# Performance work log

Measured on AMD Instinct MI355X. Metric: run time of the kernel, lower is better.

Reference implementation:

```python
import jax, jax.numpy as jnp
import numpy as np

N, E, D = 50000, 1600000, 64


def setup_inputs() -> dict:
    key = jax.random.key(0)
    ks = jax.random.split(key, 10)
    s = 1.0 / np.sqrt(D)
    return {
        "x": jax.random.normal(ks[0], (N, D), dtype=jnp.float32),
        "edge_index": jax.random.randint(ks[1], (2, E), 0, N, dtype=jnp.int64),
        "edge_weight": jax.random.uniform(ks[2], (E,), dtype=jnp.float32),
        "W_rel1": jax.random.uniform(ks[3], (D, D), jnp.float32, -s, s),
        "b_rel1": jax.random.uniform(ks[4], (D,), jnp.float32, -s, s),
        "W_root1": jax.random.uniform(ks[5], (D, D), jnp.float32, -s, s),
        "W_rel2": jax.random.uniform(ks[6], (D, D), jnp.float32, -s, s),
        "b_rel2": jax.random.uniform(ks[7], (D,), jnp.float32, -s, s),
        "W_root2": jax.random.uniform(ks[8], (D, D), jnp.float32, -s, s),
    }


def graph_conv(x, src, dst, edge_weight, W_rel, b_rel, W_root):
    # message: edge_weight * x[src]; aggregate: sum into dst
    msg = edge_weight[:, None] * x[src]                      # [E, D]
    agg = jax.ops.segment_sum(msg, dst, num_segments=x.shape[0])  # [N, D]
    return agg @ W_rel.T + b_rel + x @ W_root.T


def reference(x, edge_index, edge_weight, W_rel1, b_rel1, W_root1, W_rel2, b_rel2, W_root2):
    src, dst = edge_index[0], edge_index[1]
    h = jax.nn.relu(graph_conv(x, src, dst, edge_weight, W_rel1, b_rel1, W_root1))
    # dropout is identity in eval mode
    h = jax.nn.relu(graph_conv(h, src, dst, edge_weight, W_rel2, b_rel2, W_root2))
    return h
```

## Files before the change

### kernel.cpp

```cpp
#include <hip/hip_runtime.h>


#define NN 50000
#define DD 64
#define EE 1600000
#define NPB 64
#define NB  ((NN + NPB - 1) / NPB)
#define PAD 2560
#define CHUNK 4096
#define NC ((EE + CHUNK - 1) / CHUNK)

static_assert(NC <= 512, "colscan 2-per-thread scan covers <=512 chunks");
static_assert(NB <= 1024, "LDS cursor arrays sized for NB");

typedef __attribute__((ext_vector_type(8))) short short8;
typedef __attribute__((ext_vector_type(4))) float f32x4;

__device__ __forceinline__ unsigned short f2bf(float f) {
    unsigned u = __float_as_uint(f);
    u += 0x7FFF + ((u >> 16) & 1);
    return (unsigned short)(u >> 16);
}
__device__ __forceinline__ float bflo(unsigned u) {
    return __uint_as_float(u << 16);
}
__device__ __forceinline__ float bfhi(unsigned u) {
    return __uint_as_float(u & 0xFFFF0000u);
}
__device__ __forceinline__ unsigned char f2fp8(float f) {
    unsigned p = __builtin_amdgcn_cvt_pk_fp8_f32(f, f, 0, false);
    return (unsigned char)(p & 0xFF);
}

#define XS_STR 72
#define WS_STR 72

__device__ __forceinline__ void transform_body_f32(
    int blk, int t,
    const float* __restrict__ xin,
    const float* __restrict__ Wrel, const float* __restrict__ Wroot,
    const float* __restrict__ bias,
    unsigned char* __restrict__ Z8, unsigned short* __restrict__ Yb,
    unsigned short* Xs, unsigned short* Ws)
{
    const int node0 = blk * 64;

#pragma unroll
    for (int i = 0; i < 8; ++i) {
        int flat = i * 256 + t;
        int row  = flat >> 4;
        int c4   = flat & 15;
        const float* src = (row < 64 ? Wrel + row * 64
                                     : Wroot + (row - 64) * 64) + c4 * 4;
        float4 v = *(const float4*)src;
        unsigned short* d = &Ws[row * WS_STR + c4 * 4];
        d[0] = f2bf(v.x); d[1] = f2bf(v.y); d[2] = f2bf(v.z); d[3] = f2bf(v.w);
    }
#pragma unroll
    for (int i = 0; i < 4; ++i) {
        int flat = i * 256 + t;
        int row  = flat >> 4;
        int c4   = flat & 15;
        int node = node0 + row;
        float4 v = make_float4(0.f, 0.f, 0.f, 0.f);
        if (node < NN) v = *(const float4*)(xin + (size_t)node * 64 + c4 * 4);
        unsigned short* d = &Xs[row * XS_STR + c4 * 4];
        d[0] = f2bf(v.x); d[1] = f2bf(v.y); d[2] = f2bf(v.z); d[3] = f2bf(v.w);
    }
    __syncthreads();

    const int w    = t >> 6;
    const int lane = t & 63;
    const int l15  = lane & 15;
    const int quad = lane >> 4;

    short8 a0 = *(const short8*)&Xs[(w * 16 + l15) * XS_STR + quad * 8];
    short8 a1 = *(const short8*)&Xs[(w * 16 + l15) * XS_STR + 32 + quad * 8];

#pragma unroll
    for (int f = 0; f < 8; ++f) {
        short8 b0 = *(const short8*)&Ws[(f * 16 + l15) * WS_STR + quad * 8];
        short8 b1 = *(const short8*)&Ws[(f * 16 + l15) * WS_STR + 32 + quad * 8];
        f32x4 acc = {0.f, 0.f, 0.f, 0.f};
        acc = __builtin_amdgcn_mfma_f32_16x16x32_bf16(a0, b0, acc, 0, 0, 0);
        acc = __builtin_amdgcn_mfma_f32_16x16x32_bf16(a1, b1, acc, 0, 0, 0);
        const int col = f * 16 + l15;
#pragma unroll
        for (int r = 0; r < 4; ++r) {
            int node = node0 + w * 16 + quad * 4 + r;
            if (node < NN) {
                if (col < 64) Z8[(size_t)node * 64 + col] = f2fp8(acc[r]);
                else          Yb[(size_t)node * 64 + (col - 64)] =
                                  f2bf(acc[r] + bias[col - 64]);
            }
        }
    }
}

__global__ __launch_bounds__(256) void hist_t1_kernel(
    const int* __restrict__ ei, int* __restrict__ hist,
    const float* __restrict__ x,
    const float* __restrict__ Wrel, const float* __restrict__ Wroot,
    const float* __restrict__ bias,
    unsigned char* __restrict__ Z8, unsigned short* __restrict__ Yb)
{
    __shared__ int lh[NB];
    __shared__ unsigned short Xs[64 * XS_STR];
    __shared__ unsigned short Ws[128 * WS_STR];
    const int t = threadIdx.x;

    if (blockIdx.x < NC) {
        const int c = blockIdx.x;
        for (int b = t; b < NB; b += 256) lh[b] = 0;
        __syncthreads();
        const int base = c * CHUNK;
#pragma unroll 4
        for (int i = 0; i < CHUNK; i += 256) {
            int e = base + i + t;
            if (e < EE) atomicAdd(&lh[ei[EE + e] >> 6], 1);
        }
        __syncthreads();
        for (int b = t; b < NB; b += 256) hist[c * NB + b] = lh[b];
    } else {
        transform_body_f32(blockIdx.x - NC, t, x, Wrel, Wroot, bias,
                           Z8, Yb, Xs, Ws);
    }
}

__global__ __launch_bounds__(256) void colscan_wconv_kernel(
    const int* __restrict__ hist, int* __restrict__ offs, int* __restrict__ bsz,
    const float* __restrict__ Wrel2, const float* __restrict__ Wroot2,
    unsigned short* __restrict__ Wb2)
{
    const int t = threadIdx.x;
    if (blockIdx.x >= NB) {
        const int b2 = blockIdx.x - NB;
#pragma unroll
        for (int i = 0; i < 4; ++i) {
            int flat = b2 * 1024 + i * 256 + t;
            int row  = flat >> 4;
            int c4   = flat & 15;
            const float* src = (row < 64 ? Wrel2 + row * 64
                                         : Wroot2 + (row - 64) * 64) + c4 * 4;
            float4 v = *(const float4*)src;
            unsigned short* d = &Wb2[row * 64 + c4 * 4];
            d[0] = f2bf(v.x); d[1] = f2bf(v.y); d[2] = f2bf(v.z); d[3] = f2bf(v.w);
        }
        return;
    }
    __shared__ int part[256];
    const int b = blockIdx.x;
    const int c0 = 2 * t, c1 = 2 * t + 1;
    int h0 = (c0 < NC) ? hist[c0 * NB + b] : 0;
    int h1 = (c1 < NC) ? hist[c1 * NB + b] : 0;
    int pair = h0 + h1;
    part[t] = pair;
    __syncthreads();
    for (int off = 1; off < 256; off <<= 1) {
        int v = (t >= off) ? part[t - off] : 0;
        __syncthreads();
        part[t] += v;
        __syncthreads();
    }
    const int excl = part[t] - pair;
    if (c0 < NC) offs[c0 * NB + b] = b * PAD + excl;
    if (c1 < NC) offs[c1 * NB + b] = b * PAD + excl + h0;
    if (t == 255) bsz[b] = part[255];
}

__global__ __launch_bounds__(512) void bin_kernel(
    const int* __restrict__ ei, const float* __restrict__ ew,
    const int* __restrict__ offs, unsigned* __restrict__ epk)
{
    __shared__ int cur[NB];
    const int c = blockIdx.x, t = threadIdx.x;
    for (int b = t; b < NB; b += 512) cur[b] = offs[c * NB + b];
    __syncthreads();
    const int base = c * CHUNK;
#pragma unroll 4
    for (int i = 0; i < CHUNK; i += 512) {
        int e = base + i + t;
        if (e < EE) {
            int src = ei[e];
            int dst = ei[EE + e];
            unsigned q = (unsigned)fmaf(ew[e], 1023.0f, 0.5f);
            int pos = atomicAdd(&cur[dst >> 6], 1);
            epk[pos] = (unsigned)src | ((unsigned)(dst & 63) << 16) | (q << 22);
        }
    }
}

__global__ __launch_bounds__(512) void aggsort_t2_kernel(
    const unsigned* __restrict__ Z1,
    const uint2* __restrict__ Y4,
    const int* __restrict__ bsz,
    unsigned* __restrict__ epk,
    int* __restrict__ beg, int* __restrict__ endo,
    const unsigned short* __restrict__ Wb2,
    const float* __restrict__ bias2,
    unsigned char* __restrict__ Z8b, unsigned short* __restrict__ Yb2)
{
    __shared__ int      cnt[NPB];
    __shared__ int      nbeg[NPB];
    __shared__ int      cur[NPB];
    __shared__ unsigned stage[PAD];
    __shared__ unsigned short Xs[64 * XS_STR];
    __shared__ unsigned short Ws[128 * WS_STR];
    const int bk = blockIdx.x, t = threadIdx.x;
    const int base = bk * PAD;
    int sz = bsz[bk];
    if (sz > PAD) sz = PAD;

#pragma unroll
    for (int i = 0; i < 2; ++i) {
        int flat = i * 512 + t;
        int row  = flat >> 3;
        int c8   = flat & 7;
        *(short8*)&Ws[row * WS_STR + c8 * 8] =
            *(const short8*)&Wb2[row * 64 + c8 * 8];
    }

    if (t < NPB) cnt[t] = 0;
    __syncthreads();
    for (int i = t; i < sz; i += 512)
        atomicAdd(&cnt[(epk[base + i] >> 16) & 63], 1);
    __syncthreads();

    if (t < 64) {
        int c = cnt[t];
        int v = c;
        for (int off = 1; off < 64; off <<= 1) {
            int u = __shfl_up(v, off);
            if (t >= off) v += u;
        }
        int ex = v - c;
        nbeg[t] = ex;
        cur[t]  = ex;
        int g = bk * NPB + t;
        if (g < NN) { beg[g] = base + ex; endo[g] = base + ex + c; }
    }
    __syncthreads();

    for (int i = t; i < sz; i += 512) {
        unsigned p = epk[base + i];
        int pos = atomicAdd(&cur[(p >> 16) & 63], 1);
        float w = (float)(p >> 22) * (1.0f / 1023.0f);
        stage[pos] = (p & 0xFFFFu) | ((unsigned)f2bf(w) << 16);
    }
    __syncthreads();

    for (int i = t; i < sz; i += 512)
        epk[base + i] = stage[i];

    const int lane = t & 63;
    const int wv   = t >> 6;
    const int s = lane & 15;
    const int q = lane >> 4;

#pragma unroll
    for (int k = 0; k < 8; ++k) {
        const int n6   = wv * 8 + k;
        const int node = bk * 64 + n6;
        const int b = nbeg[n6];
        const int e = b + cnt[n6];
        const uint2 y4 = (node < NN) ? Y4[node * 16 + s] : make_uint2(0u, 0u);

        float a0 = 0.f, a1 = 0.f, a2 = 0.f, a3 = 0.f;
        int i = b;
        for (; i + 16 <= e; i += 16) {
            unsigned pA = stage[i + q];
            unsigned pB = stage[i + 4 + q];
            unsigned pC = stage[i + 8 + q];
            unsigned pD = stage[i + 12 + q];
            unsigned zA = Z1[(pA & 0xFFFF) * 16 + s];
            unsigned zB = Z1[(pB & 0xFFFF) * 16 + s];
            unsigned zC = Z1[(pC & 0xFFFF) * 16 + s];
            unsigned zD = Z1[(pD & 0xFFFF) * 16 + s];
            float wA = __uint_as_float(pA & 0xFFFF0000u);
            float wB = __uint_as_float(pB & 0xFFFF0000u);
            float wC = __uint_as_float(pC & 0xFFFF0000u);
            float wD = __uint_as_float(pD & 0xFFFF0000u);
            a0 = fmaf(wA, __builtin_amdgcn_cvt_f32_fp8(zA, 0), a0);
            a1 = fmaf(wA, __builtin_amdgcn_cvt_f32_fp8(zA, 1), a1);
            a2 = fmaf(wA, __builtin_amdgcn_cvt_f32_fp8(zA, 2), a2);
            a3 = fmaf(wA, __builtin_amdgcn_cvt_f32_fp8(zA, 3), a3);
            a0 = fmaf(wB, __builtin_amdgcn_cvt_f32_fp8(zB, 0), a0);
            a1 = fmaf(wB, __builtin_amdgcn_cvt_f32_fp8(zB, 1), a1);
            a2 = fmaf(wB, __builtin_amdgcn_cvt_f32_fp8(zB, 2), a2);
            a3 = fmaf(wB, __builtin_amdgcn_cvt_f32_fp8(zB, 3), a3);
            a0 = fmaf(wC, __builtin_amdgcn_cvt_f32_fp8(zC, 0), a0);
            a1 = fmaf(wC, __builtin_amdgcn_cvt_f32_fp8(zC, 1), a1);
            a2 = fmaf(wC, __builtin_amdgcn_cvt_f32_fp8(zC, 2), a2);
            a3 = fmaf(wC, __builtin_amdgcn_cvt_f32_fp8(zC, 3), a3);
            a0 = fmaf(wD, __builtin_amdgcn_cvt_f32_fp8(zD, 0), a0);
            a1 = fmaf(wD, __builtin_amdgcn_cvt_f32_fp8(zD, 1), a1);
            a2 = fmaf(wD, __builtin_amdgcn_cvt_f32_fp8(zD, 2), a2);
            a3 = fmaf(wD, __builtin_amdgcn_cvt_f32_fp8(zD, 3), a3);
        }
        for (; i < e; i += 4) {
            int ee = i + q;
            unsigned p = (ee < e) ? stage[ee] : 0u;
            unsigned z = Z1[(p & 0xFFFF) * 16 + s];
            float w = __uint_as_float(p & 0xFFFF0000u);
            a0 = fmaf(w, __builtin_amdgcn_cvt_f32_fp8(z, 0), a0);
            a1 = fmaf(w, __builtin_amdgcn_cvt_f32_fp8(z, 1), a1);
            a2 = fmaf(w, __builtin_amdgcn_cvt_f32_fp8(z, 2), a2);
            a3 = fmaf(w, __builtin_amdgcn_cvt_f32_fp8(z, 3), a3);
        }

        a0 += __shfl_xor(a0, 16); a0 += __shfl_xor(a0, 32);
        a1 += __shfl_xor(a1, 16); a1 += __shfl_xor(a1, 32);
        a2 += __shfl_xor(a2, 16); a2 += __shfl_xor(a2, 32);
        a3 += __shfl_xor(a3, 16); a3 += __shfl_xor(a3, 32);

        if (q == 0) {
            float r0 = fmaxf(a0 + bflo(y4.x), 0.0f);
            float r1 = fmaxf(a1 + bfhi(y4.x), 0.0f);
            float r2 = fmaxf(a2 + bflo(y4.y), 0.0f);
            float r3 = fmaxf(a3 + bfhi(y4.y), 0.0f);
            uint2 o;
            o.x = (unsigned)f2bf(r0) | ((unsigned)f2bf(r1) << 16);
            o.y = (unsigned)f2bf(r2) | ((unsigned)f2bf(r3) << 16);
            *(uint2*)&Xs[n6 * XS_STR + s * 4] = o;
        }
    }
    __syncthreads();

    {
        const int w4  = wv & 3;
        const int fh  = (wv >> 2) * 4;
        const int l15 = lane & 15;
        const int quad = lane >> 4;
        short8 A0 = *(const short8*)&Xs[(w4 * 16 + l15) * XS_STR + quad * 8];
        short8 A1 = *(const short8*)&Xs[(w4 * 16 + l15) * XS_STR + 32 + quad * 8];
#pragma unroll
        for (int f = fh; f < fh + 4; ++f) {
            short8 B0 = *(const short8*)&Ws[(f * 16 + l15) * WS_STR + quad * 8];
            short8 B1 = *(const short8*)&Ws[(f * 16 + l15) * WS_STR + 32 + quad * 8];
            f32x4 acc = {0.f, 0.f, 0.f, 0.f};
            acc = __builtin_amdgcn_mfma_f32_16x16x32_bf16(A0, B0, acc, 0, 0, 0);
            acc = __builtin_amdgcn_mfma_f32_16x16x32_bf16(A1, B1, acc, 0, 0, 0);
            const int col = f * 16 + l15;
#pragma unroll
            for (int r = 0; r < 4; ++r) {
                int node = bk * 64 + w4 * 16 + quad * 4 + r;
                if (node < NN) {
                    if (col < 64) Z8b[(size_t)node * 64 + col] = f2fp8(acc[r]);
                    else          Yb2[(size_t)node * 64 + (col - 64)] =
                                      f2bf(acc[r] + bias2[col - 64]);
                }
            }
        }
    }
}

__global__ __launch_bounds__(256) void aggregate2_kernel(
    const unsigned* __restrict__ Z1,
    const uint2* __restrict__ Y4,
    const int* __restrict__ beg, const int* __restrict__ endo,
    const unsigned* __restrict__ epk, float4* __restrict__ Hout)
{
    const int lane = threadIdx.x & 63;
    const int node = blockIdx.x * 4 + (threadIdx.x >> 6);
    if (node >= NN) return;
    const int s = lane & 15;
    const int q = lane >> 4;

    const int b = beg[node];
    const int e = endo[node];
    const uint2 y4 = Y4[node * 16 + s];

    float a0 = 0.f, a1 = 0.f, a2 = 0.f, a3 = 0.f;
    int i = b;
    for (; i + 16 <= e; i += 16) {
        unsigned pA = epk[i + q];
        unsigned pB = epk[i + 4 + q];
        unsigned pC = epk[i + 8 + q];
        unsigned pD = epk[i + 12 + q];
        unsigned zA = Z1[(pA & 0xFFFF) * 16 + s];
        unsigned zB = Z1[(pB & 0xFFFF) * 16 + s];
        unsigned zC = Z1[(pC & 0xFFFF) * 16 + s];
        unsigned zD = Z1[(pD & 0xFFFF) * 16 + s];
        float wA = __uint_as_float(pA & 0xFFFF0000u);
        float wB = __uint_as_float(pB & 0xFFFF0000u);
        float wC = __uint_as_float(pC & 0xFFFF0000u);
        float wD = __uint_as_float(pD & 0xFFFF0000u);
        a0 = fmaf(wA, __builtin_amdgcn_cvt_f32_fp8(zA, 0), a0);
        a1 = fmaf(wA, __builtin_amdgcn_cvt_f32_fp8(zA, 1), a1);
        a2 = fmaf(wA, __builtin_amdgcn_cvt_f32_fp8(zA, 2), a2);
        a3 = fmaf(wA, __builtin_amdgcn_cvt_f32_fp8(zA, 3), a3);
        a0 = fmaf(wB, __builtin_amdgcn_cvt_f32_fp8(zB, 0), a0);
        a1 = fmaf(wB, __builtin_amdgcn_cvt_f32_fp8(zB, 1), a1);
        a2 = fmaf(wB, __builtin_amdgcn_cvt_f32_fp8(zB, 2), a2);
        a3 = fmaf(wB, __builtin_amdgcn_cvt_f32_fp8(zB, 3), a3);
        a0 = fmaf(wC, __builtin_amdgcn_cvt_f32_fp8(zC, 0), a0);
        a1 = fmaf(wC, __builtin_amdgcn_cvt_f32_fp8(zC, 1), a1);
        a2 = fmaf(wC, __builtin_amdgcn_cvt_f32_fp8(zC, 2), a2);
        a3 = fmaf(wC, __builtin_amdgcn_cvt_f32_fp8(zC, 3), a3);
        a0 = fmaf(wD, __builtin_amdgcn_cvt_f32_fp8(zD, 0), a0);
        a1 = fmaf(wD, __builtin_amdgcn_cvt_f32_fp8(zD, 1), a1);
        a2 = fmaf(wD, __builtin_amdgcn_cvt_f32_fp8(zD, 2), a2);
        a3 = fmaf(wD, __builtin_amdgcn_cvt_f32_fp8(zD, 3), a3);
    }
    for (; i < e; i += 4) {
        int ee = i + q;
        unsigned p = (ee < e) ? epk[ee] : 0u;
        unsigned z = Z1[(p & 0xFFFF) * 16 + s];
        float w = __uint_as_float(p & 0xFFFF0000u);
        a0 = fmaf(w, __builtin_amdgcn_cvt_f32_fp8(z, 0), a0);
        a1 = fmaf(w, __builtin_amdgcn_cvt_f32_fp8(z, 1), a1);
        a2 = fmaf(w, __builtin_amdgcn_cvt_f32_fp8(z, 2), a2);
        a3 = fmaf(w, __builtin_amdgcn_cvt_f32_fp8(z, 3), a3);
    }

    a0 += __shfl_xor(a0, 16); a0 += __shfl_xor(a0, 32);
    a1 += __shfl_xor(a1, 16); a1 += __shfl_xor(a1, 32);
    a2 += __shfl_xor(a2, 16); a2 += __shfl_xor(a2, 32);
    a3 += __shfl_xor(a3, 16); a3 += __shfl_xor(a3, 32);

    if (q == 0) {
        float r0 = fmaxf(a0 + bflo(y4.x), 0.0f);
        float r1 = fmaxf(a1 + bfhi(y4.x), 0.0f);
        float r2 = fmaxf(a2 + bflo(y4.y), 0.0f);
        float r3 = fmaxf(a3 + bfhi(y4.y), 0.0f);
        Hout[node * 16 + s] = make_float4(r0, r1, r2, r3);
    }
}

extern "C" void kernel_launch(void* const* d_in, const int* in_sizes, int n_in,
                              void* d_out, int out_size, void* d_ws, size_t ws_size,
                              hipStream_t stream)
{
    const float* x     = (const float*)d_in[0];
    const int*   ei    = (const int*)  d_in[1];
    const float* ew    = (const float*)d_in[2];
    const float* Wrel1 = (const float*)d_in[3];
    const float* brel1 = (const float*)d_in[4];
    const float* Wroot1= (const float*)d_in[5];
    const float* Wrel2 = (const float*)d_in[6];
    const float* brel2 = (const float*)d_in[7];
    const float* Wroot2= (const float*)d_in[8];

    float* out = (float*)d_out;

    const size_t ND = (size_t)NN * DD;
    char* w = (char*)d_ws;
    unsigned char*  Z8  = (unsigned char*)w;
    unsigned short* Yb  = (unsigned short*)(w + ND);
    unsigned char*  Z8b = (unsigned char*)(w + ND * 3);
    unsigned short* Yb2 = (unsigned short*)(w + ND * 4);
    unsigned* epk = (unsigned*)(w + ND * 6);
    unsigned short* Wb2 = (unsigned short*)(w + ND * 6 + (size_t)NB * PAD * 4);
    int* bsz  = (int*)(Wb2 + 128 * 64);
    int* hist = bsz + NB;
    int* offs = hist + (size_t)NC * NB;
    int* beg  = offs + (size_t)NC * NB;
    int* endo = beg + NN;

    const int tb = (NN + 63) / 64;
    const int ab = (NN + 3) / 4;

    hist_t1_kernel<<<NC + tb, 256, 0, stream>>>(ei, hist, x, Wrel1, Wroot1,
                                                brel1, Z8, Yb);
    colscan_wconv_kernel<<<NB + 2, 256, 0, stream>>>(hist, offs, bsz,
                                                     Wrel2, Wroot2, Wb2);
    bin_kernel<<<NC, 512, 0, stream>>>(ei, ew, offs, epk);

    aggsort_t2_kernel<<<NB, 512, 0, stream>>>(
        (const unsigned*)Z8, (const uint2*)Yb, bsz, epk, beg, endo,
        Wb2, brel2, Z8b, Yb2);

    aggregate2_kernel<<<ab, 256, 0, stream>>>(
        (const unsigned*)Z8b, (const uint2*)Yb2, beg, endo, epk, (float4*)out);
}
```

Measured before the change: 178.9 us.

## Fuse layer-1 aggregation and layer-2 aggregation into one cooperative kernel with grid sync

Merges the sort/aggregate/transform kernel and the second aggregation kernel into a cooperative kernel separated by a grid-wide sync. The second aggregation reads edges from the block's LDS-sorted staging buffer instead of global memory, removing the epk write-back and the beg/endo arrays. This cuts one launch and some global traffic. The tradeoff is grid-sync cost, a residency requirement for all blocks, and less parallelism in the second phase (64 nodes per block). A fallback to the two-kernel path is kept if the cooperative launch fails.

```diff
diff --git a/kernel.cpp b/kernel.cpp
--- a/kernel.cpp
+++ b/kernel.cpp
@@ -1,4 +1,7 @@
 #include <hip/hip_runtime.h>
+#include <hip/hip_cooperative_groups.h>
+
+namespace cg = cooperative_groups;
 
 
 #define NN 50000
@@ -190,15 +193,15 @@
     }
 }
 
-__global__ __launch_bounds__(512) void aggsort_t2_kernel(
+__global__ __launch_bounds__(512, 8) void coop_kernel(
     const unsigned* __restrict__ Z1,
     const uint2* __restrict__ Y4,
     const int* __restrict__ bsz,
-    unsigned* __restrict__ epk,
-    int* __restrict__ beg, int* __restrict__ endo,
+    const unsigned* __restrict__ epk,
     const unsigned short* __restrict__ Wb2,
     const float* __restrict__ bias2,
-    unsigned char* __restrict__ Z8b, unsigned short* __restrict__ Yb2)
+    unsigned char* __restrict__ Z8b, unsigned short* __restrict__ Yb2,
+    float4* __restrict__ out)
 {
     __shared__ int      cnt[NPB];
     __shared__ int      nbeg[NPB];
@@ -236,8 +239,6 @@
         int ex = v - c;
         nbeg[t] = ex;
         cur[t]  = ex;
-        int g = bk * NPB + t;
-        if (g < NN) { beg[g] = base + ex; endo[g] = base + ex + c; }
     }
     __syncthreads();
 
@@ -248,9 +249,6 @@
         stage[pos] = (p & 0xFFFFu) | ((unsigned)f2bf(w) << 16);
     }
     __syncthreads();
-
-    for (int i = t; i < sz; i += 512)
-        epk[base + i] = stage[i];
 
     const int lane = t & 63;
     const int wv   = t >> 6;
@@ -352,11 +350,231 @@
             }
         }
     }
+
+    __threadfence();
+    cg::this_grid().sync();
+
+    const unsigned* Z2 = (const unsigned*)Z8b;
+    const uint2*    Y2 = (const uint2*)Yb2;
+#pragma unroll
+    for (int k = 0; k < 8; ++k) {
+        const int n6   = wv * 8 + k;
+        const int node = bk * 64 + n6;
+        const int b = nbeg[n6];
+        const int e = b + cnt[n6];
+        const uint2 y4 = (node < NN) ? Y2[node * 16 + s] : make_uint2(0u, 0u);
+
+        float a0 = 0.f, a1 = 0.f, a2 = 0.f, a3 = 0.f;
+        int i = b;
+        for (; i + 16 <= e; i += 16) {
+            unsigned pA = stage[i + q];
+            unsigned pB = stage[i + 4 + q];
+            unsigned pC = stage[i + 8 + q];
+            unsigned pD = stage[i + 12 + q];
+            unsigned zA = Z2[(pA & 0xFFFF) * 16 + s];
+            unsigned zB = Z2[(pB & 0xFFFF) * 16 + s];
+            unsigned zC = Z2[(pC & 0xFFFF) * 16 + s];
+            unsigned zD = Z2[(pD & 0xFFFF) * 16 + s];
+            float wA = __uint_as_float(pA & 0xFFFF0000u);
+            float wB = __uint_as_float(pB & 0xFFFF0000u);
+            float wC = __uint_as_float(pC & 0xFFFF0000u);
+            float wD = __uint_as_float(pD & 0xFFFF0000u);
+            a0 = fmaf(wA, __builtin_amdgcn_cvt_f32_fp8(zA, 0), a0);
+            a1 = fmaf(wA, __builtin_amdgcn_cvt_f32_fp8(zA, 1), a1);
+            a2 = fmaf(wA, __builtin_amdgcn_cvt_f32_fp8(zA, 2), a2);
+            a3 = fmaf(wA, __builtin_amdgcn_cvt_f32_fp8(zA, 3), a3);
+            a0 = fmaf(wB, __builtin_amdgcn_cvt_f32_fp8(zB, 0), a0);
+            a1 = fmaf(wB, __builtin_amdgcn_cvt_f32_fp8(zB, 1), a1);
+            a2 = fmaf(wB, __builtin_amdgcn_cvt_f32_fp8(zB, 2), a2);
+            a3 = fmaf(wB, __builtin_amdgcn_cvt_f32_fp8(zB, 3), a3);
+            a0 = fmaf(wC, __builtin_amdgcn_cvt_f32_fp8(zC, 0), a0);
+            a1 = fmaf(wC, __builtin_amdgcn_cvt_f32_fp8(zC, 1), a1);
+            a2 = fmaf(wC, __builtin_amdgcn_cvt_f32_fp8(zC, 2), a2);
+            a3 = fmaf(wC, __builtin_amdgcn_cvt_f32_fp8(zC, 3), a3);
+            a0 = fmaf(wD, __builtin_amdgcn_cvt_f32_fp8(zD, 0), a0);
+            a1 = fmaf(wD, __builtin_amdgcn_cvt_f32_fp8(zD, 1), a1);
+            a2 = fmaf(wD, __builtin_amdgcn_cvt_f32_fp8(zD, 2), a2);
+            a3 = fmaf(wD, __builtin_amdgcn_cvt_f32_fp8(zD, 3), a3);
+        }
+        for (; i < e; i += 4) {
+            int ee = i + q;
+            unsigned p = (ee < e) ? stage[ee] : 0u;
+            unsigned z = Z2[(p & 0xFFFF) * 16 + s];
+            float w = __uint_as_float(p & 0xFFFF0000u);
+            a0 = fmaf(w, __builtin_amdgcn_cvt_f32_fp8(z, 0), a0);
+            a1 = fmaf(w, __builtin_amdgcn_cvt_f32_fp8(z, 1), a1);
+            a2 = fmaf(w, __builtin_amdgcn_cvt_f32_fp8(z, 2), a2);
+            a3 = fmaf(w, __builtin_amdgcn_cvt_f32_fp8(z, 3), a3);
+        }
+
+        a0 += __shfl_xor(a0, 16); a0 += __shfl_xor(a0, 32);
+        a1 += __shfl_xor(a1, 16); a1 += __shfl_xor(a1, 32);
+        a2 += __shfl_xor(a2, 16); a2 += __shfl_xor(a2, 32);
+        a3 += __shfl_xor(a3, 16); a3 += __shfl_xor(a3, 32);
+
+        if (q == 0 && node < NN) {
+            float r0 = fmaxf(a0 + bflo(y4.x), 0.0f);
+            float r1 = fmaxf(a1 + bfhi(y4.x), 0.0f);
+            float r2 = fmaxf(a2 + bflo(y4.y), 0.0f);
+            float r3 = fmaxf(a3 + bfhi(y4.y), 0.0f);
+            out[node * 16 + s] = make_float4(r0, r1, r2, r3);
+        }
+    }
+}
+
+__global__ __launch_bounds__(512) void aggsort_t2_kernel(
+    const unsigned* __restrict__ Z1, const uint2* __restrict__ Y4,
+    const int* __restrict__ bsz, unsigned* __restrict__ epk,
+    int* __restrict__ beg, int* __restrict__ endo,
+    const unsigned short* __restrict__ Wb2, const float* __restrict__ bias2,
+    unsigned char* __restrict__ Z8b, unsigned short* __restrict__ Yb2)
+{
+    __shared__ int      cnt[NPB];
+    __shared__ int      nbeg[NPB];
+    __shared__ int      cur[NPB];
+    __shared__ unsigned stage[PAD];
+    __shared__ unsigned short Xs[64 * XS_STR];
+    __shared__ unsigned short Ws[128 * WS_STR];
+    const int bk = blockIdx.x, t = threadIdx.x;
+    const int base = bk * PAD;
+    int sz = bsz[bk];
+    if (sz > PAD) sz = PAD;
+
+#pragma unroll
+    for (int i = 0; i < 2; ++i) {
+        int flat = i * 512 + t;
+        int row  = flat >> 3;
+        int c8   = flat & 7;
+        *(short8*)&Ws[row * WS_STR + c8 * 8] =
+            *(const short8*)&Wb2[row * 64 + c8 * 8];
+    }
+    if (t < NPB) cnt[t] = 0;
+    __syncthreads();
+    for (int i = t; i < sz; i += 512)
+        atomicAdd(&cnt[(epk[base + i] >> 16) & 63], 1);
+    __syncthreads();
+    if (t < 64) {
+        int c = cnt[t];
+        int v = c;
+        for (int off = 1; off < 64; off <<= 1) {
+            int u = __shfl_up(v, off);
+            if (t >= off) v += u;
+        }
+        int ex = v - c;
+        nbeg[t] = ex; cur[t] = ex;
+        int g = bk * NPB + t;
+        if (g < NN) { beg[g] = base + ex; endo[g] = base + ex + c; }
+    }
+    __syncthreads();
+    for (int i = t; i < sz; i += 512) {
+        unsigned p = epk[base + i];
+        int pos = atomicAdd(&cur[(p >> 16) & 63], 1);
+        float w = (float)(p >> 22) * (1.0f / 1023.0f);
+        stage[pos] = (p & 0xFFFFu) | ((unsigned)f2bf(w) << 16);
+    }
+    __syncthreads();
+    for (int i = t; i < sz; i += 512) epk[base + i] = stage[i];
+
+    const int lane = t & 63;
+    const int wv   = t >> 6;
+    const int s = lane & 15;
+    const int q = lane >> 4;
+
+#pragma unroll
+    for (int k = 0; k < 8; ++k) {
+        const int n6   = wv * 8 + k;
+        const int node = bk * 64 + n6;
+        const int b = nbeg[n6];
+        const int e = b + cnt[n6];
+        const uint2 y4 = (node < NN) ? Y4[node * 16 + s] : make_uint2(0u, 0u);
+        float a0 = 0.f, a1 = 0.f, a2 = 0.f, a3 = 0.f;
+        int i = b;
+        for (; i + 16 <= e; i += 16) {
+            unsigned pA = stage[i + q];
+            unsigned pB = stage[i + 4 + q];
+            unsigned pC = stage[i + 8 + q];
+            unsigned pD = stage[i + 12 + q];
+            unsigned zA = Z1[(pA & 0xFFFF) * 16 + s];
+            unsigned zB = Z1[(pB & 0xFFFF) * 16 + s];
+            unsigned zC = Z1[(pC & 0xFFFF) * 16 + s];
+            unsigned zD = Z1[(pD & 0xFFFF) * 16 + s];
+            float wA = __uint_as_float(pA & 0xFFFF0000u);
+            float wB = __uint_as_float(pB & 0xFFFF0000u);
+            float wC = __uint_as_float(pC & 0xFFFF0000u);
+            float wD = __uint_as_float(pD & 0xFFFF0000u);
+            a0 = fmaf(wA, __builtin_amdgcn_cvt_f32_fp8(zA, 0), a0);
+            a1 = fmaf(wA, __builtin_amdgcn_cvt_f32_fp8(zA, 1), a1);
+            a2 = fmaf(wA, __builtin_amdgcn_cvt_f32_fp8(zA, 2), a2);
+            a3 = fmaf(wA, __builtin_amdgcn_cvt_f32_fp8(zA, 3), a3);
+            a0 = fmaf(wB, __builtin_amdgcn_cvt_f32_fp8(zB, 0), a0);
+            a1 = fmaf(wB, __builtin_amdgcn_cvt_f32_fp8(zB, 1), a1);
+            a2 = fmaf(wB, __builtin_amdgcn_cvt_f32_fp8(zB, 2), a2);
+            a3 = fmaf(wB, __builtin_amdgcn_cvt_f32_fp8(zB, 3), a3);
+            a0 = fmaf(wC, __builtin_amdgcn_cvt_f32_fp8(zC, 0), a0);
+            a1 = fmaf(wC, __builtin_amdgcn_cvt_f32_fp8(zC, 1), a1);
+            a2 = fmaf(wC, __builtin_amdgcn_cvt_f32_fp8(zC, 2), a2);
+            a3 = fmaf(wC, __builtin_amdgcn_cvt_f32_fp8(zC, 3), a3);
+            a0 = fmaf(wD, __builtin_amdgcn_cvt_f32_fp8(zD, 0), a0);
+            a1 = fmaf(wD, __builtin_amdgcn_cvt_f32_fp8(zD, 1), a1);
+            a2 = fmaf(wD, __builtin_amdgcn_cvt_f32_fp8(zD, 2), a2);
+            a3 = fmaf(wD, __builtin_amdgcn_cvt_f32_fp8(zD, 3), a3);
+        }
+        for (; i < e; i += 4) {
+            int ee = i + q;
+            unsigned p = (ee < e) ? stage[ee] : 0u;
+            unsigned z = Z1[(p & 0xFFFF) * 16 + s];
+            float w = __uint_as_float(p & 0xFFFF0000u);
+            a0 = fmaf(w, __builtin_amdgcn_cvt_f32_fp8(z, 0), a0);
+            a1 = fmaf(w, __builtin_amdgcn_cvt_f32_fp8(z, 1), a1);
+            a2 = fmaf(w, __builtin_amdgcn_cvt_f32_fp8(z, 2), a2);
+            a3 = fmaf(w, __builtin_amdgcn_cvt_f32_fp8(z, 3), a3);
+        }
+        a0 += __shfl_xor(a0, 16); a0 += __shfl_xor(a0, 32);
+        a1 += __shfl_xor(a1, 16); a1 += __shfl_xor(a1, 32);
+        a2 += __shfl_xor(a2, 16); a2 += __shfl_xor(a2, 32);
+        a3 += __shfl_xor(a3, 16); a3 += __shfl_xor(a3, 32);
+        if (q == 0) {
+            float r0 = fmaxf(a0 + bflo(y4.x), 0.0f);
+            float r1 = fmaxf(a1 + bfhi(y4.x), 0.0f);
+            float r2 = fmaxf(a2 + bflo(y4.y), 0.0f);
+            float r3 = fmaxf(a3 + bfhi(y4.y), 0.0f);
+            uint2 o;
+            o.x = (unsigned)f2bf(r0) | ((unsigned)f2bf(r1) << 16);
+            o.y = (unsigned)f2bf(r2) | ((unsigned)f2bf(r3) << 16);
+            *(uint2*)&Xs[n6 * XS_STR + s * 4] = o;
+        }
+    }
+    __syncthreads();
+    {
+        const int w4  = wv & 3;
+        const int fh  = (wv >> 2) * 4;
+        const int l15 = lane & 15;
+        const int quad = lane >> 4;
+        short8 A0 = *(const short8*)&Xs[(w4 * 16 + l15) * XS_STR + quad * 8];
+        short8 A1 = *(const short8*)&Xs[(w4 * 16 + l15) * XS_STR + 32 + quad * 8];
+#pragma unroll
+        for (int f = fh; f < fh + 4; ++f) {
+            short8 B0 = *(const short8*)&Ws[(f * 16 + l15) * WS_STR + quad * 8];
+            short8 B1 = *(const short8*)&Ws[(f * 16 + l15) * WS_STR + 32 + quad * 8];
+            f32x4 acc = {0.f, 0.f, 0.f, 0.f};
+            acc = __builtin_amdgcn_mfma_f32_16x16x32_bf16(A0, B0, acc, 0, 0, 0);
+            acc = __builtin_amdgcn_mfma_f32_16x16x32_bf16(A1, B1, acc, 0, 0, 0);
+            const int col = f * 16 + l15;
+#pragma unroll
+            for (int r = 0; r < 4; ++r) {
+                int node = bk * 64 + w4 * 16 + quad * 4 + r;
+                if (node < NN) {
+                    if (col < 64) Z8b[(size_t)node * 64 + col] = f2fp8(acc[r]);
+                    else          Yb2[(size_t)node * 64 + (col - 64)] =
+                                      f2bf(acc[r] + bias2[col - 64]);
+                }
+            }
+        }
+    }
 }
 
 __global__ __launch_bounds__(256) void aggregate2_kernel(
-    const unsigned* __restrict__ Z1,
-    const uint2* __restrict__ Y4,
+    const unsigned* __restrict__ Z1, const uint2* __restrict__ Y4,
     const int* __restrict__ beg, const int* __restrict__ endo,
     const unsigned* __restrict__ epk, float4* __restrict__ Hout)
 {
@@ -365,11 +583,9 @@
     if (node >= NN) return;
     const int s = lane & 15;
     const int q = lane >> 4;
-
     const int b = beg[node];
     const int e = endo[node];
     const uint2 y4 = Y4[node * 16 + s];
-
     float a0 = 0.f, a1 = 0.f, a2 = 0.f, a3 = 0.f;
     int i = b;
     for (; i + 16 <= e; i += 16) {
@@ -412,12 +628,10 @@
         a2 = fmaf(w, __builtin_amdgcn_cvt_f32_fp8(z, 2), a2);
         a3 = fmaf(w, __builtin_amdgcn_cvt_f32_fp8(z, 3), a3);
     }
-
     a0 += __shfl_xor(a0, 16); a0 += __shfl_xor(a0, 32);
     a1 += __shfl_xor(a1, 16); a1 += __shfl_xor(a1, 32);
     a2 += __shfl_xor(a2, 16); a2 += __shfl_xor(a2, 32);
     a3 += __shfl_xor(a3, 16); a3 += __shfl_xor(a3, 32);
-
     if (q == 0) {
         float r0 = fmaxf(a0 + bflo(y4.x), 0.0f);
         float r1 = fmaxf(a1 + bfhi(y4.x), 0.0f);
@@ -466,10 +680,25 @@
                                                      Wrel2, Wroot2, Wb2);
     bin_kernel<<<NC, 512, 0, stream>>>(ei, ew, offs, epk);
 
-    aggsort_t2_kernel<<<NB, 512, 0, stream>>>(
-        (const unsigned*)Z8, (const uint2*)Yb, bsz, epk, beg, endo,
-        Wb2, brel2, Z8b, Yb2);
-
-    aggregate2_kernel<<<ab, 256, 0, stream>>>(
-        (const unsigned*)Z8b, (const uint2*)Yb2, beg, endo, epk, (float4*)out);
-}
+    const unsigned*       Z1p  = (const unsigned*)Z8;
+    const uint2*          Y4p  = (const uint2*)Yb;
+    const int*            bszp = bsz;
+    const unsigned*       epkp = epk;
+    const unsigned short* Wb2p = Wb2;
+    const float*          b2p  = brel2;
+    unsigned char*        Z8bp = Z8b;
+    unsigned short*       Yb2p = Yb2;
+    float4*               outp = (float4*)out;
+    void* args[] = {&Z1p, &Y4p, &bszp, &epkp, &Wb2p, &b2p, &Z8bp, &Yb2p, &outp};
+    hipError_t cerr = hipLaunchCooperativeKernel(
+        (const void*)coop_kernel, dim3(NB), dim3(512), args, 0, stream);
+    if (cerr != hipSuccess) {
+        (void)hipGetLastError();
+        aggsort_t2_kernel<<<NB, 512, 0, stream>>>(
+            (const unsigned*)Z8, (const uint2*)Yb, bsz, epk, beg, endo,
+            Wb2, brel2, Z8b, Yb2);
+        aggregate2_kernel<<<ab, 256, 0, stream>>>(
+            (const unsigned*)Z8b, (const uint2*)Yb2, beg, endo, epk,
+            (float4*)out);
+    }
+}
```

Result: slower. 469.0 us (+162.2%).

## Fuse histogram, scan and binning into one kernel using global atomic cursors

Applied to the files above, without the earlier changes.

Replaces the hist / column-scan / bin three-kernel pipeline with a single build kernel. Each chunk computes its local histogram, reserves space per bucket with a global atomicAdd on a zeroed cursor array, then scatters packed edges immediately. The layer-1 transform and the W2 bf16 conversion are folded into the same launch with 512-thread blocks. This removes two launches and the hist/offs global round trips, but the order of edges within a bucket becomes nondeterministic, which can change floating-point summation order.

```diff
diff --git a/kernel.cpp b/kernel.cpp
--- a/kernel.cpp
+++ b/kernel.cpp
@@ -10,7 +10,6 @@
 #define CHUNK 4096
 #define NC ((EE + CHUNK - 1) / CHUNK)
 
-static_assert(NC <= 512, "colscan 2-per-thread scan covers <=512 chunks");
 static_assert(NB <= 1024, "LDS cursor arrays sized for NB");
 
 typedef __attribute__((ext_vector_type(8))) short short8;
@@ -35,157 +34,126 @@
 #define XS_STR 72
 #define WS_STR 72
 
-__device__ __forceinline__ void transform_body_f32(
-    int blk, int t,
-    const float* __restrict__ xin,
-    const float* __restrict__ Wrel, const float* __restrict__ Wroot,
-    const float* __restrict__ bias,
+__global__ __launch_bounds__(256) void zero_kernel(int* __restrict__ gcur)
+{
+    int i = blockIdx.x * 256 + threadIdx.x;
+    if (i < NB) gcur[i] = 0;
+}
+
+__global__ __launch_bounds__(512) void build_t1_kernel(
+    const int* __restrict__ ei, const float* __restrict__ ew,
+    int* __restrict__ gcur, unsigned* __restrict__ epk,
+    const float* __restrict__ x,
+    const float* __restrict__ Wrel1, const float* __restrict__ Wroot1,
+    const float* __restrict__ bias1,
     unsigned char* __restrict__ Z8, unsigned short* __restrict__ Yb,
-    unsigned short* Xs, unsigned short* Ws)
-{
-    const int node0 = blk * 64;
-
-#pragma unroll
-    for (int i = 0; i < 8; ++i) {
-        int flat = i * 256 + t;
-        int row  = flat >> 4;
-        int c4   = flat & 15;
-        const float* src = (row < 64 ? Wrel + row * 64
-                                     : Wroot + (row - 64) * 64) + c4 * 4;
-        float4 v = *(const float4*)src;
-        unsigned short* d = &Ws[row * WS_STR + c4 * 4];
-        d[0] = f2bf(v.x); d[1] = f2bf(v.y); d[2] = f2bf(v.z); d[3] = f2bf(v.w);
-    }
-#pragma unroll
-    for (int i = 0; i < 4; ++i) {
-        int flat = i * 256 + t;
-        int row  = flat >> 4;
-        int c4   = flat & 15;
-        int node = node0 + row;
-        float4 v = make_float4(0.f, 0.f, 0.f, 0.f);
-        if (node < NN) v = *(const float4*)(xin + (size_t)node * 64 + c4 * 4);
-        unsigned short* d = &Xs[row * XS_STR + c4 * 4];
-        d[0] = f2bf(v.x); d[1] = f2bf(v.y); d[2] = f2bf(v.z); d[3] = f2bf(v.w);
-    }
-    __syncthreads();
-
-    const int w    = t >> 6;
-    const int lane = t & 63;
-    const int l15  = lane & 15;
-    const int quad = lane >> 4;
-
-    short8 a0 = *(const short8*)&Xs[(w * 16 + l15) * XS_STR + quad * 8];
-    short8 a1 = *(const short8*)&Xs[(w * 16 + l15) * XS_STR + 32 + quad * 8];
-
-#pragma unroll
-    for (int f = 0; f < 8; ++f) {
-        short8 b0 = *(const short8*)&Ws[(f * 16 + l15) * WS_STR + quad * 8];
-        short8 b1 = *(const short8*)&Ws[(f * 16 + l15) * WS_STR + 32 + quad * 8];
-        f32x4 acc = {0.f, 0.f, 0.f, 0.f};
-        acc = __builtin_amdgcn_mfma_f32_16x16x32_bf16(a0, b0, acc, 0, 0, 0);
-        acc = __builtin_amdgcn_mfma_f32_16x16x32_bf16(a1, b1, acc, 0, 0, 0);
-        const int col = f * 16 + l15;
-#pragma unroll
-        for (int r = 0; r < 4; ++r) {
-            int node = node0 + w * 16 + quad * 4 + r;
-            if (node < NN) {
-                if (col < 64) Z8[(size_t)node * 64 + col] = f2fp8(acc[r]);
-                else          Yb[(size_t)node * 64 + (col - 64)] =
-                                  f2bf(acc[r] + bias[col - 64]);
-            }
-        }
-    }
-}
-
-__global__ __launch_bounds__(256) void hist_t1_kernel(
-    const int* __restrict__ ei, int* __restrict__ hist,
-    const float* __restrict__ x,
-    const float* __restrict__ Wrel, const float* __restrict__ Wroot,
-    const float* __restrict__ bias,
-    unsigned char* __restrict__ Z8, unsigned short* __restrict__ Yb)
+    const float* __restrict__ Wrel2, const float* __restrict__ Wroot2,
+    unsigned short* __restrict__ Wb2)
 {
     __shared__ int lh[NB];
+    __shared__ int cur[NB];
     __shared__ unsigned short Xs[64 * XS_STR];
     __shared__ unsigned short Ws[128 * WS_STR];
     const int t = threadIdx.x;
 
     if (blockIdx.x < NC) {
         const int c = blockIdx.x;
-        for (int b = t; b < NB; b += 256) lh[b] = 0;
+        for (int b = t; b < NB; b += 512) lh[b] = 0;
         __syncthreads();
         const int base = c * CHUNK;
 #pragma unroll 4
-        for (int i = 0; i < CHUNK; i += 256) {
+        for (int i = 0; i < CHUNK; i += 512) {
             int e = base + i + t;
             if (e < EE) atomicAdd(&lh[ei[EE + e] >> 6], 1);
         }
         __syncthreads();
-        for (int b = t; b < NB; b += 256) hist[c * NB + b] = lh[b];
+        for (int b = t; b < NB; b += 512) {
+            int h = lh[b];
+            if (h) cur[b] = b * PAD + atomicAdd(&gcur[b], h);
+        }
+        __syncthreads();
+#pragma unroll 4
+        for (int i = 0; i < CHUNK; i += 512) {
+            int e = base + i + t;
+            if (e < EE) {
+                int src = ei[e];
+                int dst = ei[EE + e];
+                unsigned q = (unsigned)fmaf(ew[e], 1023.0f, 0.5f);
+                int pos = atomicAdd(&cur[dst >> 6], 1);
+                epk[pos] = (unsigned)src | ((unsigned)(dst & 63) << 16)
+                                         | (q << 22);
+            }
+        }
+    } else if (blockIdx.x < NC + (NN + 63) / 64) {
+        const int blk = blockIdx.x - NC;
+        const int node0 = blk * 64;
+
+#pragma unroll
+        for (int i = 0; i < 4; ++i) {
+            int flat = i * 512 + t;
+            int row  = flat >> 4;
+            int c4   = flat & 15;
+            const float* src = (row < 64 ? Wrel1 + row * 64
+                                         : Wroot1 + (row - 64) * 64) + c4 * 4;
+            float4 v = *(const float4*)src;
+            unsigned short* d = &Ws[row * WS_STR + c4 * 4];
+            d[0] = f2bf(v.x); d[1] = f2bf(v.y);
+            d[2] = f2bf(v.z); d[3] = f2bf(v.w);
+        }
+#pragma unroll
+        for (int i = 0; i < 2; ++i) {
+            int flat = i * 512 + t;
+            int row  = flat >> 4;
+            int c4   = flat & 15;
+            int node = node0 + row;
+            float4 v = make_float4(0.f, 0.f, 0.f, 0.f);
+            if (node < NN) v = *(const float4*)(x + (size_t)node * 64 + c4 * 4);
+            unsigned short* d = &Xs[row * XS_STR + c4 * 4];
+            d[0] = f2bf(v.x); d[1] = f2bf(v.y);
+            d[2] = f2bf(v.z); d[3] = f2bf(v.w);
+        }
+        __syncthreads();
+
+        const int lane = t & 63;
+        const int wv   = t >> 6;
+        const int w4   = wv & 3;
+        const int fh   = (wv >> 2) * 4;
+        const int l15  = lane & 15;
+        const int quad = lane >> 4;
+
+        short8 A0 = *(const short8*)&Xs[(w4 * 16 + l15) * XS_STR + quad * 8];
+        short8 A1 = *(const short8*)&Xs[(w4 * 16 + l15) * XS_STR + 32 + quad * 8];
+#pragma unroll
+        for (int f = fh; f < fh + 4; ++f) {
+            short8 B0 = *(const short8*)&Ws[(f * 16 + l15) * WS_STR + quad * 8];
+            short8 B1 = *(const short8*)&Ws[(f * 16 + l15) * WS_STR + 32 + quad * 8];
+            f32x4 acc = {0.f, 0.f, 0.f, 0.f};
+            acc = __builtin_amdgcn_mfma_f32_16x16x32_bf16(A0, B0, acc, 0, 0, 0);
+            acc = __builtin_amdgcn_mfma_f32_16x16x32_bf16(A1, B1, acc, 0, 0, 0);
+            const int col = f * 16 + l15;
+#pragma unroll
+            for (int r = 0; r < 4; ++r) {
+                int node = node0 + w4 * 16 + quad * 4 + r;
+                if (node < NN) {
+                    if (col < 64) Z8[(size_t)node * 64 + col] = f2fp8(acc[r]);
+                    else          Yb[(size_t)node * 64 + (col - 64)] =
+                                      f2bf(acc[r] + bias1[col - 64]);
+                }
+            }
+        }
     } else {
-        transform_body_f32(blockIdx.x - NC, t, x, Wrel, Wroot, bias,
-                           Z8, Yb, Xs, Ws);
-    }
-}
-
-__global__ __launch_bounds__(256) void colscan_wconv_kernel(
-    const int* __restrict__ hist, int* __restrict__ offs, int* __restrict__ bsz,
-    const float* __restrict__ Wrel2, const float* __restrict__ Wroot2,
-    unsigned short* __restrict__ Wb2)
-{
-    const int t = threadIdx.x;
-    if (blockIdx.x >= NB) {
-        const int b2 = blockIdx.x - NB;
-#pragma unroll
-        for (int i = 0; i < 4; ++i) {
-            int flat = b2 * 1024 + i * 256 + t;
+        const int b2 = blockIdx.x - NC - (NN + 63) / 64;
+#pragma unroll
+        for (int i = 0; i < 2; ++i) {
+            int flat = b2 * 1024 + i * 512 + t;
             int row  = flat >> 4;
             int c4   = flat & 15;
             const float* src = (row < 64 ? Wrel2 + row * 64
                                          : Wroot2 + (row - 64) * 64) + c4 * 4;
             float4 v = *(const float4*)src;
             unsigned short* d = &Wb2[row * 64 + c4 * 4];
-            d[0] = f2bf(v.x); d[1] = f2bf(v.y); d[2] = f2bf(v.z); d[3] = f2bf(v.w);
-        }
-        return;
-    }
-    __shared__ int part[256];
-    const int b = blockIdx.x;
-    const int c0 = 2 * t, c1 = 2 * t + 1;
-    int h0 = (c0 < NC) ? hist[c0 * NB + b] : 0;
-    int h1 = (c1 < NC) ? hist[c1 * NB + b] : 0;
-    int pair = h0 + h1;
-    part[t] = pair;
-    __syncthreads();
-    for (int off = 1; off < 256; off <<= 1) {
-        int v = (t >= off) ? part[t - off] : 0;
-        __syncthreads();
-        part[t] += v;
-        __syncthreads();
-    }
-    const int excl = part[t] - pair;
-    if (c0 < NC) offs[c0 * NB + b] = b * PAD + excl;
-    if (c1 < NC) offs[c1 * NB + b] = b * PAD + excl + h0;
-    if (t == 255) bsz[b] = part[255];
-}
-
-__global__ __launch_bounds__(512) void bin_kernel(
-    const int* __restrict__ ei, const float* __restrict__ ew,
-    const int* __restrict__ offs, unsigned* __restrict__ epk)
-{
-    __shared__ int cur[NB];
-    const int c = blockIdx.x, t = threadIdx.x;
-    for (int b = t; b < NB; b += 512) cur[b] = offs[c * NB + b];
-    __syncthreads();
-    const int base = c * CHUNK;
-#pragma unroll 4
-    for (int i = 0; i < CHUNK; i += 512) {
-        int e = base + i + t;
-        if (e < EE) {
-            int src = ei[e];
-            int dst = ei[EE + e];
-            unsigned q = (unsigned)fmaf(ew[e], 1023.0f, 0.5f);
-            int pos = atomicAdd(&cur[dst >> 6], 1);
-            epk[pos] = (unsigned)src | ((unsigned)(dst & 63) << 16) | (q << 22);
+            d[0] = f2bf(v.x); d[1] = f2bf(v.y);
+            d[2] = f2bf(v.z); d[3] = f2bf(v.w);
         }
     }
 }
@@ -451,23 +419,21 @@
     unsigned short* Yb2 = (unsigned short*)(w + ND * 4);
     unsigned* epk = (unsigned*)(w + ND * 6);
     unsigned short* Wb2 = (unsigned short*)(w + ND * 6 + (size_t)NB * PAD * 4);
-    int* bsz  = (int*)(Wb2 + 128 * 64);
-    int* hist = bsz + NB;
-    int* offs = hist + (size_t)NC * NB;
-    int* beg  = offs + (size_t)NC * NB;
+    int* gcur = (int*)(Wb2 + 128 * 64);
+    int* beg  = gcur + NB;
     int* endo = beg + NN;
 
     const int tb = (NN + 63) / 64;
     const int ab = (NN + 3) / 4;
 
-    hist_t1_kernel<<<NC + tb, 256, 0, stream>>>(ei, hist, x, Wrel1, Wroot1,
-                                                brel1, Z8, Yb);
-    colscan_wconv_kernel<<<NB + 2, 256, 0, stream>>>(hist, offs, bsz,
-                                                     Wrel2, Wroot2, Wb2);
-    bin_kernel<<<NC, 512, 0, stream>>>(ei, ew, offs, epk);
+    zero_kernel<<<(NB + 255) / 256, 256, 0, stream>>>(gcur);
+
+    build_t1_kernel<<<NC + tb + 2, 512, 0, stream>>>(
+        ei, ew, gcur, epk, x, Wrel1, Wroot1, brel1, Z8, Yb,
+        Wrel2, Wroot2, Wb2);
 
     aggsort_t2_kernel<<<NB, 512, 0, stream>>>(
-        (const unsigned*)Z8, (const uint2*)Yb, bsz, epk, beg, endo,
+        (const unsigned*)Z8, (const uint2*)Yb, gcur, epk, beg, endo,
         Wb2, brel2, Z8b, Yb2);
 
     aggregate2_kernel<<<ab, 256, 0, stream>>>(
```

New measurement: 173.2 us. -3.2%, faster.
